# Performance work log

Hardware: AMD Instinct MI355X
Metric: run time of the kernel (lower is better)

The kernel has to match this reference:

```python
import jax, jax.numpy as jnp
import numpy as np

B, S = 4, 2048          # batch, seq tokens
D_IN, D_HID = 1280, 2048  # from CAMERAMOE emb_size / d_inner
E, K = 8, 2             # num_experts, top_k
LN_EPS = 1e-6


def setup_inputs() -> dict:
    key = jax.random.key(0)
    ks = jax.random.split(key, 8)
    rn = lambda k, shp, sc=1.0: jax.random.normal(k, shp, dtype=jnp.float32) * sc
    return {
        "x": rn(ks[0], (B, S, D_IN)),
        "noise": rn(ks[1], (B, S, E)),          # the randn_like draw, made explicit
        "wr": rn(ks[2], (D_IN, E), 0.02), "br": jnp.zeros((E,), jnp.float32),
        "wn": rn(ks[3], (D_IN, E), 0.02), "bn": jnp.zeros((E,), jnp.float32),
        "w1": rn(ks[4], (E, D_IN, D_HID), 0.02), "b1": jnp.zeros((E, D_HID), jnp.float32),
        "w2": rn(ks[5], (E, D_HID, D_IN), 0.02), "b2": jnp.zeros((E, D_IN), jnp.float32),
        "gamma": jnp.ones((E, D_IN), jnp.float32), "beta": jnp.zeros((E, D_IN), jnp.float32),
    }


def reference(x, noise, wr, br, wn, bn, w1, b1, w2, b2, gamma, beta):
    # --- NoisyTopkRouter ---
    logits = x @ wr + br                                  # [B,S,E]
    noise_logits = x @ wn + bn                            # [B,S,E]
    noisy = logits + noise * jax.nn.softplus(noise_logits)
    _, idx = jax.lax.top_k(noisy, K)                      # [B,S,K]
    sel = jax.nn.one_hot(idx, E, dtype=bool).any(axis=-2) # [B,S,E] selected-expert mask
    sparse_logits = jnp.where(sel, noisy, -jnp.inf)       # scatter of top-k logits into -inf
    gates = jax.nn.softmax(sparse_logits, axis=-1)        # zeros for non-selected experts

    # --- SparseMoE combine (gate-weighted sum over experts; gate==0 masks out
    # non-selected tokens, matching the torch masked gather/scatter-add math) ---
    h = jax.nn.relu(jnp.einsum('bsd,edh->ebsh', x, w1) + b1[:, None, None, :])
    y = jnp.einsum('ebsh,ehd->ebsd', h, w2) + b2[:, None, None, :]
    y = y + x                                             # residual (broadcast over E)
    mu = y.mean(axis=-1, keepdims=True)
    var = y.var(axis=-1, keepdims=True)
    y = (y - mu) * jax.lax.rsqrt(var + LN_EPS)
    y = y * gamma[:, None, None, :] + beta[:, None, None, :]
    return jnp.einsum('ebsd,bse->bsd', y, gates)          # [B,S,D_IN]
```

## Files before the change

### kernel.cpp

```cpp
#include <hip/hip_runtime.h>
#include <stdint.h>

typedef unsigned short u16;
typedef __attribute__((ext_vector_type(8))) short short8;
typedef __attribute__((ext_vector_type(4))) float f32x4;
typedef __attribute__((ext_vector_type(4))) float float4v;
typedef __attribute__((ext_vector_type(4))) unsigned short us4;
typedef __attribute__((ext_vector_type(8))) unsigned short us8;

#define TOK   8192
#define DIN   1280
#define DHID  2048
#define NEXP  8
#define RCAP  17408
#define MT128 136

#define TRBLK1 5120
#define TRBLK2 5120
#define RTRBLK 1024
#define G1BLKS 2176

__device__ __forceinline__ float bf2f(u16 u) {
  union { unsigned int i; float f; } v; v.i = ((unsigned int)u) << 16; return v.f;
}
__device__ __forceinline__ u16 f2bf(float f) {
  union { float f; unsigned int i; } v; v.f = f;
  unsigned int x = v.i;
  return (u16)((x + 0x7fffu + ((x >> 16) & 1u)) >> 16);
}

__device__ __forceinline__ void gload16(const u16* g, void* lds) {
  __builtin_amdgcn_global_load_lds(
      (const __attribute__((address_space(1))) unsigned int*)g,
      (__attribute__((address_space(3))) unsigned int*)lds, 16, 0, 0);
}

__device__ __forceinline__ void tr_tile(u16* ldsT, const float* in, u16* outp,
                                        int RK, int CN, int rb, int cb)
{
  int tid = threadIdx.x, w = tid >> 6, lane = tid & 63;
  {
    const float* src = in + (size_t)(rb + lane) * CN + cb + w * 16;
    u16 val[16];
    #pragma unroll
    for (int k = 0; k < 4; k++) {
      float4v v = *(const float4v*)(src + k * 4);
      #pragma unroll
      for (int j = 0; j < 4; j++) val[k * 4 + j] = f2bf(v[j]);
    }
    #pragma unroll
    for (int j = 0; j < 16; j++)
      ldsT[(w * 16 + j) * 72 + lane] = val[j];
  }
  __syncthreads();
  {
    int oc = tid >> 2, rch = (tid & 3) * 16;
    const u16* s = &ldsT[oc * 72 + rch];
    u16* d = outp + (size_t)(cb + oc) * RK + rb + rch;
    *(us8*)(d)     = *(const us8*)(s);
    *(us8*)(d + 8) = *(const us8*)(s + 8);
  }
}

__global__ __launch_bounds__(256) void routertr_k(
    const float* __restrict__ w1, u16* __restrict__ W1t,
    const float* __restrict__ x, const float* __restrict__ noise,
    const float* __restrict__ wr, const float* __restrict__ br,
    const float* __restrict__ wn, const float* __restrict__ bn,
    int* __restrict__ topk_e, float* __restrict__ topk_g)
{
  __shared__ u16 ldsT[64 * 72];
  int id = blockIdx.x;

  if (id >= RTRBLK) {
    int id2 = id - RTRBLK;
    int e = id2 / 640, r = id2 % 640;
    int rb = (r >> 5) * 64, cb = (r & 31) * 64;
    tr_tile(ldsT, w1 + (size_t)e * DIN * DHID, W1t + (size_t)e * DIN * DHID,
            DIN, DHID, rb, cb);
    return;
  }

  int w = threadIdx.x >> 6, lane = threadIdx.x & 63;
  int t0 = id * 8 + w * 2;
  int h = lane & 1, dl = lane >> 1;
  const float* xA = x + (size_t)t0 * DIN;
  const float* xB = xA + DIN;

  float ra[4], na[4], rb2[4], nb2[4];
  #pragma unroll
  for (int j = 0; j < 4; j++) { ra[j] = 0.f; na[j] = 0.f; rb2[j] = 0.f; nb2[j] = 0.f; }

  #pragma unroll 4
  for (int d0 = 0; d0 < DIN; d0 += 32) {
    int d = d0 + dl;
    float4v wrv = *(const float4v*)(wr + (size_t)d * 8 + h * 4);
    float4v wnv = *(const float4v*)(wn + (size_t)d * 8 + h * 4);
    float xa = xA[d], xb = xB[d];
    #pragma unroll
    for (int j = 0; j < 4; j++) {
      ra[j]  += xa * wrv[j]; na[j]  += xa * wnv[j];
      rb2[j] += xb * wrv[j]; nb2[j] += xb * wnv[j];
    }
  }
  #pragma unroll
  for (int off = 2; off < 64; off <<= 1) {
    #pragma unroll
    for (int j = 0; j < 4; j++) {
      ra[j]  += __shfl_xor(ra[j],  off);
      na[j]  += __shfl_xor(na[j],  off);
      rb2[j] += __shfl_xor(rb2[j], off);
      nb2[j] += __shfl_xor(nb2[j], off);
    }
  }
  float raO[4], naO[4], rbO[4], nbO[4];
  #pragma unroll
  for (int j = 0; j < 4; j++) {
    raO[j] = __shfl_xor(ra[j], 1);
    naO[j] = __shfl_xor(na[j], 1);
    rbO[j] = __shfl_xor(rb2[j], 1);
    nbO[j] = __shfl_xor(nb2[j], 1);
  }
  if (lane == 0) {
    #pragma unroll
    for (int tt = 0; tt < 2; tt++) {
      int t = t0 + tt;
      float noisy[8];
      #pragma unroll
      for (int j = 0; j < 4; j++) {
        float lg0 = (tt ? rb2[j] : ra[j]) + br[j];
        float nl0 = (tt ? nb2[j] : na[j]) + bn[j];
        float lg1 = (tt ? rbO[j] : raO[j]) + br[4 + j];
        float nl1 = (tt ? nbO[j] : nbO[j]) + bn[4 + j];
        nl1 = (tt ? nbO[j] : naO[j]) + bn[4 + j];
        float sp0 = (nl0 > 0.f) ? nl0 + log1pf(expf(-nl0)) : log1pf(expf(nl0));
        float sp1 = (nl1 > 0.f) ? nl1 + log1pf(expf(-nl1)) : log1pf(expf(nl1));
        noisy[j]     = lg0 + noise[(size_t)t * 8 + j] * sp0;
        noisy[4 + j] = lg1 + noise[(size_t)t * 8 + 4 + j] * sp1;
      }
      int e0 = 0; float v0 = noisy[0];
      #pragma unroll
      for (int e = 1; e < 8; e++) if (noisy[e] > v0) { v0 = noisy[e]; e0 = e; }
      int e1 = -1; float v1 = -1e30f;
      #pragma unroll
      for (int e = 0; e < 8; e++) if (e != e0 && noisy[e] > v1) { v1 = noisy[e]; e1 = e; }
      float g0 = 1.f / (1.f + expf(v1 - v0));
      topk_e[2*t] = e0; topk_e[2*t+1] = e1;
      topk_g[2*t] = g0; topk_g[2*t+1] = 1.f - g0;
    }
  }
}

__global__ __launch_bounds__(1024) void scan_k(
    const int* __restrict__ topk_e, int* __restrict__ rowmap, int* __restrict__ aoffs)
{
  __shared__ int cnt[1024][8];
  __shared__ int tot[8];
  __shared__ int base[8];
  int tid = threadIdx.x;
  int ebuf[16];
  #pragma unroll
  for (int j = 0; j < 16; j++) ebuf[j] = topk_e[tid * 16 + j];
  int c0=0,c1=0,c2=0,c3=0,c4=0,c5=0,c6=0,c7=0;
  #pragma unroll
  for (int j = 0; j < 16; j++) {
    int e = ebuf[j];
    c0 += (e==0); c1 += (e==1); c2 += (e==2); c3 += (e==3);
    c4 += (e==4); c5 += (e==5); c6 += (e==6); c7 += (e==7);
  }
  cnt[tid][0]=c0; cnt[tid][1]=c1; cnt[tid][2]=c2; cnt[tid][3]=c3;
  cnt[tid][4]=c4; cnt[tid][5]=c5; cnt[tid][6]=c6; cnt[tid][7]=c7;
  __syncthreads();

  int w = tid >> 6, lane = tid & 63;
  if (w < 8) {
    int e = w;
    int s[16]; int run = 0;
    #pragma unroll
    for (int j = 0; j < 16; j++) { s[j] = run; run += cnt[lane*16+j][e]; }
    int inc = run;
    for (int off = 1; off < 64; off <<= 1) {
      int v = __shfl_up(inc, off);
      if (lane >= off) inc += v;
    }
    int lane_excl = inc - run;
    #pragma unroll
    for (int j = 0; j < 16; j++) cnt[lane*16+j][e] = lane_excl + s[j];
    if (lane == 63) tot[e] = inc;
  }
  __syncthreads();
  if (tid == 0) {
    int a = 0;
    for (int e = 0; e < 8; e++) { base[e] = a; aoffs[e] = a; a += (tot[e] + 127) & ~127; }
    aoffs[8] = a;
  }
  __syncthreads();
  int o0 = base[0]+cnt[tid][0], o1 = base[1]+cnt[tid][1], o2 = base[2]+cnt[tid][2],
      o3 = base[3]+cnt[tid][3], o4 = base[4]+cnt[tid][4], o5 = base[5]+cnt[tid][5],
      o6 = base[6]+cnt[tid][6], o7 = base[7]+cnt[tid][7];
  #pragma unroll
  for (int j = 0; j < 16; j++) {
    int e = ebuf[j];
    int row = o0;
    row = (e==1) ? o1 : row; row = (e==2) ? o2 : row; row = (e==3) ? o3 : row;
    row = (e==4) ? o4 : row; row = (e==5) ? o5 : row; row = (e==6) ? o6 : row;
    row = (e==7) ? o7 : row;
    o0 += (e==0); o1 += (e==1); o2 += (e==2); o3 += (e==3);
    o4 += (e==4); o5 += (e==5); o6 += (e==6); o7 += (e==7);
    rowmap[tid * 16 + j] = row;
  }
}

__global__ __launch_bounds__(256) void gather_k(
    const float* __restrict__ x, const int* __restrict__ rowmap,
    u16* __restrict__ Xe)
{
  int w = threadIdx.x >> 6, lane = threadIdx.x & 63;
  int t = blockIdx.x * 4 + w;
  int r0 = rowmap[2*t], r1 = rowmap[2*t+1];
  const float4v* xs = (const float4v*)(x + (size_t)t * DIN);
  us4* d0 = (us4*)(Xe + (size_t)r0 * DIN);
  us4* d1 = (us4*)(Xe + (size_t)r1 * DIN);
  #pragma unroll
  for (int i = 0; i < DIN / 4 / 64; i++) {
    int q = i * 64 + lane;
    float4v v = xs[q];
    us4 o;
    #pragma unroll
    for (int j = 0; j < 4; j++) o[j] = f2bf(v[j]);
    d0[q] = o;
    d1[q] = o;
  }
}

__device__ __forceinline__ void gemm128_body(
    u16* sm, const u16* A, const u16* Bt, const float* bias, u16* Out,
    const int* aoffs, int K, int N, int relu, int bx, int by)
{
  int row0 = by * 128;
  if (row0 >= aoffs[NEXP]) return;
  int e = 0;
  #pragma unroll
  for (int i = 0; i < NEXP; i++) if (row0 >= aoffs[i + 1]) e = i + 1;
  int ncol0 = bx * 128;
  const u16* Ab = A + (size_t)row0 * K;
  const u16* Bb = Bt + ((size_t)e * N + ncol0) * K;

  int tid = threadIdx.x, w = tid >> 6, lane = tid & 63;
  int wr = w >> 1, wc = w & 1;
  int l15 = lane & 15, l4 = lane >> 4;
  int xorv = (l15 & 7) << 3;

  int srow[4], skc[4];
  #pragma unroll
  for (int q = 0; q < 4; q++) {
    int cd = q * 256 + tid;
    int cs = cd ^ ((cd >> 3) & 7);
    srow[q] = cs >> 3;
    skc[q]  = (cs & 7) * 8;
  }
  int ldsw = w * 1024;

  f32x4 acc[4][4];
  #pragma unroll
  for (int m = 0; m < 4; m++)
    #pragma unroll
    for (int n = 0; n < 4; n++) acc[m][n] = (f32x4){0.f, 0.f, 0.f, 0.f};

  short8 a[4][2], b0[2][2], b1[2][2];

#define STAGE_A(T, BUF) do {                                                  \
    char* d_ = (char*)sm + (BUF) * 32768;                                     \
    int ko_ = (T) * 64;                                                       \
    _Pragma("unroll")                                                         \
    for (int q = 0; q < 4; q++)                                               \
      gload16(Ab + (size_t)srow[q] * K + ko_ + skc[q], d_ + q*4096 + ldsw);   \
  } while (0)
#define STAGE_B(T, BUF) do {                                                  \
    char* d_ = (char*)sm + (BUF) * 32768 + 16384;                             \
    int ko_ = (T) * 64;                                                       \
    _Pragma("unroll")                                                         \
    for (int q = 0; q < 4; q++)                                               \
      gload16(Bb + (size_t)srow[q] * K + ko_ + skc[q], d_ + q*4096 + ldsw);   \
  } while (0)
#define RD_A() do {                                                           \
    _Pragma("unroll")                                                         \
    for (int m = 0; m < 4; m++)                                               \
      _Pragma("unroll")                                                       \
      for (int ks = 0; ks < 2; ks++) {                                        \
        int r_ = wr*64 + m*16 + l15;                                          \
        a[m][ks] = *(const short8*)&smA[(r_*64 + ks*32 + l4*8) ^ xorv];       \
      }                                                                       \
  } while (0)
#define RD_B(DST, NH) do {                                                    \
    _Pragma("unroll")                                                         \
    for (int n = 0; n < 2; n++)                                               \
      _Pragma("unroll")                                                       \
      for (int ks = 0; ks < 2; ks++) {                                        \
        int r_ = wc*64 + (NH)*32 + n*16 + l15;                                \
        DST[n][ks] = *(const short8*)&smB[(r_*64 + ks*32 + l4*8) ^ xorv];     \
      }                                                                       \
  } while (0)
#define MFMA16(NH, BB) do {                                                   \
    _Pragma("unroll")                                                         \
    for (int m = 0; m < 4; m++)                                               \
      _Pragma("unroll")                                                       \
      for (int n = 0; n < 2; n++)                                             \
        _Pragma("unroll")                                                     \
        for (int ks = 0; ks < 2; ks++)                                        \
          acc[m][(NH)*2+n] = __builtin_amdgcn_mfma_f32_16x16x32_bf16(         \
              a[m][ks], BB[n][ks], acc[m][(NH)*2+n], 0, 0, 0);                \
  } while (0)
#define BAR __builtin_amdgcn_s_barrier()

  int NT = K >> 6;
  STAGE_A(0, 0);
  STAGE_B(0, 0);
  STAGE_A(1, 1);
  STAGE_B(1, 1);
  asm volatile("s_waitcnt vmcnt(8)" ::: "memory");
  BAR;

  for (int t = 0; t < NT; ++t) {
    int buf = t & 1;
    const u16* smA = sm + buf * 16384;
    const u16* smB = smA + 8192;
    RD_A();
    RD_B(b0, 0);
    RD_B(b1, 1);
    asm volatile("s_waitcnt lgkmcnt(0)" ::: "memory");
    BAR;
    if (t + 2 < NT) {
      STAGE_A(t + 2, buf);
      STAGE_B(t + 2, buf);
    }
    __builtin_amdgcn_s_setprio(1);
    MFMA16(0, b0);
    MFMA16(1, b1);
    __builtin_amdgcn_s_setprio(0);
    if (t + 2 < NT) {
      asm volatile("s_waitcnt vmcnt(8)" ::: "memory");
    } else if (t + 1 < NT) {
      asm volatile("s_waitcnt vmcnt(0)" ::: "memory");
    }
    BAR;
  }
#undef STAGE_A
#undef STAGE_B
#undef RD_A
#undef RD_B
#undef MFMA16
#undef BAR

  #pragma unroll
  for (int in = 0; in < 4; in++) {
    int c = ncol0 + wc * 64 + in * 16 + l15;
    float bv = bias[(size_t)e * N + c];
    #pragma unroll
    for (int im = 0; im < 4; im++) {
      int rb = row0 + wr * 64 + im * 16 + l4 * 4;
      #pragma unroll
      for (int j = 0; j < 4; j++) {
        float v = acc[im][in][j] + bv;
        if (relu) v = fmaxf(v, 0.f);
        Out[(size_t)(rb + j) * N + c] = f2bf(v);
      }
    }
  }
}

__global__ __launch_bounds__(256, 2) void gemm1tr_k(
    const u16* __restrict__ A, const u16* __restrict__ Bt,
    const float* __restrict__ bias, u16* __restrict__ Out,
    const int* __restrict__ aoffs,
    const float* __restrict__ w2, u16* __restrict__ W2t)
{
  extern __shared__ u16 sm[];
  int id = blockIdx.x;
  if (id < G1BLKS) {
    int per = G1BLKS >> 3;
    int sid = (id & 7) * per + (id >> 3);
    gemm128_body(sm, A, Bt, bias, Out, aoffs, DIN, DHID, 1, sid % 16, sid / 16);
    return;
  }
  int id2 = id - G1BLKS;
  int e = id2 / 640, r = id2 % 640;
  int rb = (r / 20) * 64, cb = (r % 20) * 64;
  tr_tile(sm, w2 + (size_t)e * DHID * DIN, W2t + (size_t)e * DHID * DIN,
          DHID, DIN, rb, cb);
}

__global__ __launch_bounds__(256, 2) void gemm128_k(
    const u16* __restrict__ A, const u16* __restrict__ Bt,
    const float* __restrict__ bias, u16* __restrict__ Out,
    const int* __restrict__ aoffs, int K, int N, int relu)
{
  extern __shared__ u16 sm[];
  int nwgx = gridDim.x;
  int id = blockIdx.y * nwgx + blockIdx.x;
  int per = (nwgx * gridDim.y) >> 3;
  int sid = (id & 7) * per + (id >> 3);
  gemm128_body(sm, A, Bt, bias, Out, aoffs, K, N, relu, sid % nwgx, sid / nwgx);
}

__global__ __launch_bounds__(256) void ln_k(
    const float* __restrict__ x, const u16* __restrict__ Y,
    const int* __restrict__ rowmap, const int* __restrict__ topk_e,
    const float* __restrict__ topk_g, const float* __restrict__ gamma,
    const float* __restrict__ beta, float* __restrict__ out)
{
  int w = threadIdx.x >> 6, lane = threadIdx.x & 63;
  int t = blockIdx.x * 4 + w;
  int r0 = rowmap[2*t], r1 = rowmap[2*t+1];
  int e0 = topk_e[2*t], e1 = topk_e[2*t+1];
  float g0 = topk_g[2*t], g1 = topk_g[2*t+1];
  const float4v* xt = (const float4v*)(x + (size_t)t * DIN);
  const us4* y0p = (const us4*)(Y + (size_t)r0 * DIN);
  const us4* y1p = (const us4*)(Y + (size_t)r1 * DIN);
  float4v v0[5], v1[5];
  float s0 = 0.f, q0 = 0.f, s1 = 0.f, q1 = 0.f;
  #pragma unroll
  for (int i = 0; i < 5; i++) {
    int q = i * 64 + lane;
    float4v xv = xt[q];
    us4 ya = y0p[q], yb = y1p[q];
    #pragma unroll
    for (int j = 0; j < 4; j++) {
      float aa = xv[j] + bf2f(ya[j]);
      float bb = xv[j] + bf2f(yb[j]);
      v0[i][j] = aa; v1[i][j] = bb;
      s0 += aa; q0 += aa * aa; s1 += bb; q1 += bb * bb;
    }
  }
  #pragma unroll
  for (int off = 32; off; off >>= 1) {
    s0 += __shfl_xor(s0, off); q0 += __shfl_xor(q0, off);
    s1 += __shfl_xor(s1, off); q1 += __shfl_xor(q1, off);
  }
  const float inv = 1.f / DIN;
  float mu0 = s0 * inv, mu1 = s1 * inv;
  float rs0 = rsqrtf(fmaxf(q0 * inv - mu0 * mu0, 0.f) + 1e-6f);
  float rs1 = rsqrtf(fmaxf(q1 * inv - mu1 * mu1, 0.f) + 1e-6f);
  const float4v* ga0 = (const float4v*)(gamma + (size_t)e0 * DIN);
  const float4v* be0 = (const float4v*)(beta  + (size_t)e0 * DIN);
  const float4v* ga1 = (const float4v*)(gamma + (size_t)e1 * DIN);
  const float4v* be1 = (const float4v*)(beta  + (size_t)e1 * DIN);
  float4v* op = (float4v*)(out + (size_t)t * DIN);
  #pragma unroll
  for (int i = 0; i < 5; i++) {
    int q = i * 64 + lane;
    float4v gA = ga0[q], bA = be0[q], gB = ga1[q], bB = be1[q];
    float4v o;
    #pragma unroll
    for (int j = 0; j < 4; j++) {
      float n0 = (v0[i][j] - mu0) * rs0 * gA[j] + bA[j];
      float n1 = (v1[i][j] - mu1) * rs1 * gB[j] + bB[j];
      o[j] = g0 * n0 + g1 * n1;
    }
    op[q] = o;
  }
}

extern "C" void kernel_launch(void* const* d_in, const int* in_sizes, int n_in,
                              void* d_out, int out_size, void* d_ws, size_t ws_size,
                              hipStream_t stream)
{
  const float* x     = (const float*)d_in[0];
  const float* noise = (const float*)d_in[1];
  const float* wr    = (const float*)d_in[2];
  const float* br    = (const float*)d_in[3];
  const float* wn    = (const float*)d_in[4];
  const float* bn    = (const float*)d_in[5];
  const float* w1    = (const float*)d_in[6];
  const float* b1    = (const float*)d_in[7];
  const float* w2    = (const float*)d_in[8];
  const float* b2    = (const float*)d_in[9];
  const float* gamma = (const float*)d_in[10];
  const float* beta  = (const float*)d_in[11];
  float* out = (float*)d_out;
  char* ws = (char*)d_ws;

  int*   aoffs   = (int*)(ws + 128);
  int*   rowmap  = (int*)(ws + 4096);
  int*   topk_e  = (int*)(ws + 4096 + 65536);
  float* topk_g  = (float*)(ws + 4096 + 2 * 65536);

  const size_t XE_OFF   = (size_t)1 << 20;
  const size_t XE_BYTES = (size_t)RCAP * DIN * 2;
  const size_t H_BYTES  = (size_t)RCAP * DHID * 2;
  const size_t WT_BYTES = (size_t)NEXP * DHID * DIN * 2;
  u16* Xe  = (u16*)(ws + XE_OFF);
  u16* Hb  = (u16*)(ws + XE_OFF + XE_BYTES);
  u16* Yb  = Xe;
  u16* W1t = (u16*)(ws + XE_OFF + XE_BYTES + H_BYTES);
  u16* W2t = (u16*)(ws + XE_OFF + XE_BYTES + H_BYTES + WT_BYTES);

  routertr_k<<<RTRBLK + TRBLK1, 256, 0, stream>>>(
      w1, W1t, x, noise, wr, br, wn, bn, topk_e, topk_g);
  scan_k<<<1, 1024, 0, stream>>>(topk_e, rowmap, aoffs);
  gather_k<<<TOK/4, 256, 0, stream>>>(x, rowmap, Xe);
  gemm1tr_k<<<G1BLKS + TRBLK2, 256, 65536, stream>>>(Xe, W1t, b1, Hb, aoffs, w2, W2t);
  gemm128_k<<<dim3(DIN/128, MT128), 256, 65536, stream>>>(Hb, W2t, b2, Yb, aoffs, DHID, DIN, 0);
  ln_k<<<TOK/4, 256, 0, stream>>>(x, Yb, rowmap, topk_e, topk_g, gamma, beta, out);
}
```

Before: 330.4 us.

## Replace gather kernel with indirect A-row loads in first expert GEMM

```diff
diff --git a/kernel.cpp b/kernel.cpp
--- a/kernel.cpp
+++ b/kernel.cpp
@@ -18,6 +18,7 @@
 #define TRBLK1 5120
 #define TRBLK2 5120
 #define RTRBLK 1024
+#define XBBLK  2048
 #define G1BLKS 2176
 
 __device__ __forceinline__ float bf2f(u16 u) {
@@ -67,21 +68,37 @@
     const float* __restrict__ x, const float* __restrict__ noise,
     const float* __restrict__ wr, const float* __restrict__ br,
     const float* __restrict__ wn, const float* __restrict__ bn,
-    int* __restrict__ topk_e, float* __restrict__ topk_g)
+    int* __restrict__ topk_e, float* __restrict__ topk_g,
+    u16* __restrict__ Xbf)
 {
   __shared__ u16 ldsT[64 * 72];
   int id = blockIdx.x;
-
-  if (id >= RTRBLK) {
-    int id2 = id - RTRBLK;
+  int w = threadIdx.x >> 6, lane = threadIdx.x & 63;
+
+  if (id >= RTRBLK + XBBLK) {
+    int id2 = id - (RTRBLK + XBBLK);
     int e = id2 / 640, r = id2 % 640;
     int rb = (r >> 5) * 64, cb = (r & 31) * 64;
     tr_tile(ldsT, w1 + (size_t)e * DIN * DHID, W1t + (size_t)e * DIN * DHID,
             DIN, DHID, rb, cb);
     return;
   }
-
-  int w = threadIdx.x >> 6, lane = threadIdx.x & 63;
+  if (id >= RTRBLK) {
+    int t = (id - RTRBLK) * 4 + w;
+    const float4v* xs = (const float4v*)(x + (size_t)t * DIN);
+    us4* d0 = (us4*)(Xbf + (size_t)t * DIN);
+    #pragma unroll
+    for (int i = 0; i < DIN / 4 / 64; i++) {
+      int q = i * 64 + lane;
+      float4v v = xs[q];
+      us4 o;
+      #pragma unroll
+      for (int j = 0; j < 4; j++) o[j] = f2bf(v[j]);
+      d0[q] = o;
+    }
+    return;
+  }
+
   int t0 = id * 8 + w * 2;
   int h = lane & 1, dl = lane >> 1;
   const float* xA = x + (size_t)t0 * DIN;
@@ -131,8 +148,7 @@
         float lg0 = (tt ? rb2[j] : ra[j]) + br[j];
         float nl0 = (tt ? nb2[j] : na[j]) + bn[j];
         float lg1 = (tt ? rbO[j] : raO[j]) + br[4 + j];
-        float nl1 = (tt ? nbO[j] : nbO[j]) + bn[4 + j];
-        nl1 = (tt ? nbO[j] : naO[j]) + bn[4 + j];
+        float nl1 = (tt ? nbO[j] : naO[j]) + bn[4 + j];
         float sp0 = (nl0 > 0.f) ? nl0 + log1pf(expf(-nl0)) : log1pf(expf(nl0));
         float sp1 = (nl1 > 0.f) ? nl1 + log1pf(expf(-nl1)) : log1pf(expf(nl1));
         noisy[j]     = lg0 + noise[(size_t)t * 8 + j] * sp0;
@@ -152,7 +168,8 @@
 }
 
 __global__ __launch_bounds__(1024) void scan_k(
-    const int* __restrict__ topk_e, int* __restrict__ rowmap, int* __restrict__ aoffs)
+    const int* __restrict__ topk_e, int* __restrict__ rowmap,
+    int* __restrict__ tokmap, int* __restrict__ aoffs)
 {
   __shared__ int cnt[1024][8];
   __shared__ int tot[8];
@@ -195,11 +212,17 @@
     aoffs[8] = a;
   }
   __syncthreads();
+  if (w < 8) {
+    int e = w;
+    int region = (tot[e] + 127) & ~127;
+    for (int r = tot[e] + lane; r < region; r += 64) tokmap[base[e] + r] = 0;
+  }
   int o0 = base[0]+cnt[tid][0], o1 = base[1]+cnt[tid][1], o2 = base[2]+cnt[tid][2],
       o3 = base[3]+cnt[tid][3], o4 = base[4]+cnt[tid][4], o5 = base[5]+cnt[tid][5],
       o6 = base[6]+cnt[tid][6], o7 = base[7]+cnt[tid][7];
   #pragma unroll
   for (int j = 0; j < 16; j++) {
+    int p = tid * 16 + j;
     int e = ebuf[j];
     int row = o0;
     row = (e==1) ? o1 : row; row = (e==2) ? o2 : row; row = (e==3) ? o3 : row;
@@ -207,34 +230,15 @@
     row = (e==7) ? o7 : row;
     o0 += (e==0); o1 += (e==1); o2 += (e==2); o3 += (e==3);
     o4 += (e==4); o5 += (e==5); o6 += (e==6); o7 += (e==7);
-    rowmap[tid * 16 + j] = row;
-  }
-}
-
-__global__ __launch_bounds__(256) void gather_k(
-    const float* __restrict__ x, const int* __restrict__ rowmap,
-    u16* __restrict__ Xe)
-{
-  int w = threadIdx.x >> 6, lane = threadIdx.x & 63;
-  int t = blockIdx.x * 4 + w;
-  int r0 = rowmap[2*t], r1 = rowmap[2*t+1];
-  const float4v* xs = (const float4v*)(x + (size_t)t * DIN);
-  us4* d0 = (us4*)(Xe + (size_t)r0 * DIN);
-  us4* d1 = (us4*)(Xe + (size_t)r1 * DIN);
-  #pragma unroll
-  for (int i = 0; i < DIN / 4 / 64; i++) {
-    int q = i * 64 + lane;
-    float4v v = xs[q];
-    us4 o;
-    #pragma unroll
-    for (int j = 0; j < 4; j++) o[j] = f2bf(v[j]);
-    d0[q] = o;
-    d1[q] = o;
-  }
-}
-
+    rowmap[p] = row;
+    tokmap[row] = p >> 1;
+  }
+}
+
+template<bool IND>
 __device__ __forceinline__ void gemm128_body(
-    u16* sm, const u16* A, const u16* Bt, const float* bias, u16* Out,
+    u16* sm, const u16* A, const int* tokmap, const u16* Bt,
+    const float* bias, u16* Out,
     const int* aoffs, int K, int N, int relu, int bx, int by)
 {
   int row0 = by * 128;
@@ -243,7 +247,7 @@
   #pragma unroll
   for (int i = 0; i < NEXP; i++) if (row0 >= aoffs[i + 1]) e = i + 1;
   int ncol0 = bx * 128;
-  const u16* Ab = A + (size_t)row0 * K;
+  const u16* Ab = IND ? A : A + (size_t)row0 * K;
   const u16* Bb = Bt + ((size_t)e * N + ncol0) * K;
 
   int tid = threadIdx.x, w = tid >> 6, lane = tid & 63;
@@ -251,13 +255,15 @@
   int l15 = lane & 15, l4 = lane >> 4;
   int xorv = (l15 & 7) << 3;
 
-  int srow[4], skc[4];
+  size_t arow[4]; int skc[4]; int srowb[4];
   #pragma unroll
   for (int q = 0; q < 4; q++) {
     int cd = q * 256 + tid;
     int cs = cd ^ ((cd >> 3) & 7);
-    srow[q] = cs >> 3;
+    int sr = cs >> 3;
+    srowb[q] = sr;
     skc[q]  = (cs & 7) * 8;
+    arow[q] = IND ? (size_t)tokmap[row0 + sr] : (size_t)sr;
   }
   int ldsw = w * 1024;
 
@@ -274,14 +280,14 @@
     int ko_ = (T) * 64;                                                       \
     _Pragma("unroll")                                                         \
     for (int q = 0; q < 4; q++)                                               \
-      gload16(Ab + (size_t)srow[q] * K + ko_ + skc[q], d_ + q*4096 + ldsw);   \
+      gload16(Ab + arow[q] * K + ko_ + skc[q], d_ + q*4096 + ldsw);           \
   } while (0)
 #define STAGE_B(T, BUF) do {                                                  \
     char* d_ = (char*)sm + (BUF) * 32768 + 16384;                             \
     int ko_ = (T) * 64;                                                       \
     _Pragma("unroll")                                                         \
     for (int q = 0; q < 4; q++)                                               \
-      gload16(Bb + (size_t)srow[q] * K + ko_ + skc[q], d_ + q*4096 + ldsw);   \
+      gload16(Bb + (size_t)srowb[q] * K + ko_ + skc[q], d_ + q*4096 + ldsw);  \
   } while (0)
 #define RD_A() do {                                                           \
     _Pragma("unroll")                                                         \
@@ -370,9 +376,9 @@
 }
 
 __global__ __launch_bounds__(256, 2) void gemm1tr_k(
-    const u16* __restrict__ A, const u16* __restrict__ Bt,
+    const u16* __restrict__ Xbf, const u16* __restrict__ Bt,
     const float* __restrict__ bias, u16* __restrict__ Out,
-    const int* __restrict__ aoffs,
+    const int* __restrict__ aoffs, const int* __restrict__ tokmap,
     const float* __restrict__ w2, u16* __restrict__ W2t)
 {
   extern __shared__ u16 sm[];
@@ -380,7 +386,8 @@
   if (id < G1BLKS) {
     int per = G1BLKS >> 3;
     int sid = (id & 7) * per + (id >> 3);
-    gemm128_body(sm, A, Bt, bias, Out, aoffs, DIN, DHID, 1, sid % 16, sid / 16);
+    gemm128_body<true>(sm, Xbf, tokmap, Bt, bias, Out, aoffs, DIN, DHID, 1,
+                       sid % 16, sid / 16);
     return;
   }
   int id2 = id - G1BLKS;
@@ -400,7 +407,8 @@
   int id = blockIdx.y * nwgx + blockIdx.x;
   int per = (nwgx * gridDim.y) >> 3;
   int sid = (id & 7) * per + (id >> 3);
-  gemm128_body(sm, A, Bt, bias, Out, aoffs, K, N, relu, sid % nwgx, sid / nwgx);
+  gemm128_body<false>(sm, A, nullptr, Bt, bias, Out, aoffs, K, N, relu,
+                      sid % nwgx, sid / nwgx);
 }
 
 __global__ __launch_bounds__(256) void ln_k(
@@ -484,22 +492,23 @@
   int*   rowmap  = (int*)(ws + 4096);
   int*   topk_e  = (int*)(ws + 4096 + 65536);
   float* topk_g  = (float*)(ws + 4096 + 2 * 65536);
-
-  const size_t XE_OFF   = (size_t)1 << 20;
-  const size_t XE_BYTES = (size_t)RCAP * DIN * 2;
+  int*   tokmap  = (int*)(ws + 4096 + 3 * 65536);
+
+  const size_t XB_OFF   = (size_t)1 << 20;
+  const size_t XB_BYTES = (size_t)TOK * DIN * 2;
   const size_t H_BYTES  = (size_t)RCAP * DHID * 2;
+  const size_t Y_BYTES  = (size_t)RCAP * DIN * 2;
   const size_t WT_BYTES = (size_t)NEXP * DHID * DIN * 2;
-  u16* Xe  = (u16*)(ws + XE_OFF);
-  u16* Hb  = (u16*)(ws + XE_OFF + XE_BYTES);
-  u16* Yb  = Xe;
-  u16* W1t = (u16*)(ws + XE_OFF + XE_BYTES + H_BYTES);
-  u16* W2t = (u16*)(ws + XE_OFF + XE_BYTES + H_BYTES + WT_BYTES);
-
-  routertr_k<<<RTRBLK + TRBLK1, 256, 0, stream>>>(
-      w1, W1t, x, noise, wr, br, wn, bn, topk_e, topk_g);
-  scan_k<<<1, 1024, 0, stream>>>(topk_e, rowmap, aoffs);
-  gather_k<<<TOK/4, 256, 0, stream>>>(x, rowmap, Xe);
-  gemm1tr_k<<<G1BLKS + TRBLK2, 256, 65536, stream>>>(Xe, W1t, b1, Hb, aoffs, w2, W2t);
+  u16* Xbf = (u16*)(ws + XB_OFF);
+  u16* Hb  = (u16*)(ws + XB_OFF + XB_BYTES);
+  u16* Yb  = (u16*)(ws + XB_OFF + XB_BYTES + H_BYTES);
+  u16* W1t = (u16*)(ws + XB_OFF + XB_BYTES + H_BYTES + Y_BYTES);
+  u16* W2t = (u16*)(ws + XB_OFF + XB_BYTES + H_BYTES + Y_BYTES + WT_BYTES);
+
+  routertr_k<<<RTRBLK + XBBLK + TRBLK1, 256, 0, stream>>>(
+      w1, W1t, x, noise, wr, br, wn, bn, topk_e, topk_g, Xbf);
+  scan_k<<<1, 1024, 0, stream>>>(topk_e, rowmap, tokmap, aoffs);
+  gemm1tr_k<<<G1BLKS + TRBLK2, 256, 65536, stream>>>(Xbf, W1t, b1, Hb, aoffs, tokmap, w2, W2t);
   gemm128_k<<<dim3(DIN/128, MT128), 256, 65536, stream>>>(Hb, W2t, b2, Yb, aoffs, DHID, DIN, 0);
   ln_k<<<TOK/4, 256, 0, stream>>>(x, Yb, rowmap, topk_e, topk_g, gamma, beta, out);
 }
```

After: 321.9 us, median of 2. 2.6% less time.
